# Optimization experiments

Hardware: AMD Instinct MI355X
Metric: run time of the kernel (lower is better)

## Reference

```python
import jax, jax.numpy as jnp
import numpy as np

H = 1024   # hidden_size
NH = 16    # num heads
DH = H // NH
L = 2      # attention levels
E = 8      # experts
F = 4 * H  # expert FFN hidden
B = 2
S = 1024
EPS = 1e-5
TOPK = 2
STD = 0.02


def setup_inputs() -> dict:
    key = jax.random.key(0)
    ks = jax.random.split(key, 12)
    def n(k, shp):
        return jax.random.normal(k, shp, jnp.float32) * STD
    return {
        "hidden_states": jax.random.normal(ks[0], (B, S, H), jnp.float32),
        "attention_mask": jnp.ones((B, S), jnp.int32),
        "ln1_g": jnp.ones((H,), jnp.float32), "ln1_b": jnp.zeros((H,), jnp.float32),
        "ln2_g": jnp.ones((H,), jnp.float32), "ln2_b": jnp.zeros((H,), jnp.float32),
        "Wq": n(ks[1], (L, H, H)), "Wk": n(ks[2], (L, H, H)),
        "Wv": n(ks[3], (L, H, H)), "Wo": n(ks[4], (L, H, H)),
        "bq": jnp.zeros((L, H), jnp.float32), "bk": jnp.zeros((L, H), jnp.float32),
        "bv": jnp.zeros((L, H), jnp.float32), "bo": jnp.zeros((L, H), jnp.float32),
        "level_logits": n(ks[5], (L,)),
        "Wr": n(ks[6], (H, E)), "br": jnp.zeros((E,), jnp.float32),
        "W1": n(ks[7], (E, H, F)), "b1": jnp.zeros((E, F), jnp.float32),
        "W2": n(ks[8], (E, F, H)), "b2": jnp.zeros((E, H), jnp.float32),
    }


def _ln(x, g, b):
    m = x.mean(-1, keepdims=True)
    v = x.var(-1, keepdims=True)
    return (x - m) * jax.lax.rsqrt(v + EPS) * g + b


def _mla(x, mask_f, Wq, Wk, Wv, Wo, bq, bk, bv, bo, level_logits):
    # Multi-level attention: one MHA per level, softmax-combined over levels.
    b_, s_, _ = x.shape
    def proj(W, bias):
        y = jnp.einsum('bsh,lhd->lbsd', x, W) + bias[:, None, None, :]
        return y.reshape(L, b_, s_, NH, DH)
    q, k, v = proj(Wq, bq), proj(Wk, bk), proj(Wv, bv)
    scores = jnp.einsum('lbqnd,lbknd->lbnqk', q, k) / np.float32(np.sqrt(DH))
    bias = (1.0 - mask_f)[None, :, None, None, :] * jnp.float32(-1e9)  # key-side mask
    attn = jax.nn.softmax(scores + bias, axis=-1)
    ctx = jnp.einsum('lbnqk,lbknd->lbqnd', attn, v).reshape(L, b_, s_, H)
    out = jnp.einsum('lbsh,lhd->lbsd', ctx, Wo) + bo[:, None, None, :]
    w = jax.nn.softmax(level_logits)
    return jnp.einsum('l,lbsd->bsd', w, out)


def _moe(x, Wr, br, W1, b1, W2, b2):
    # Top-2 softmax router with renormalized gates; dense expert compute,
    # sparse combine (math-equivalent to dispatch/combine without dropping).
    logits = x @ Wr + br                                  # [B,S,E]
    probs = jax.nn.softmax(logits, axis=-1)
    topv, topi = jax.lax.top_k(probs, TOPK)               # [B,S,K]
    gates = topv / topv.sum(-1, keepdims=True)
    combine = jnp.sum(jax.nn.one_hot(topi, E, dtype=x.dtype) * gates[..., None], axis=-2)  # [B,S,E]
    h = jax.nn.gelu(jnp.einsum('bsh,ehf->besf', x, W1) + b1[None, :, None, :])
    y = jnp.einsum('besf,efh->besh', h, W2) + b2[None, :, None, :]
    return jnp.einsum('bse,besh->bsh', combine, y), logits


def reference(hidden_states, attention_mask, ln1_g, ln1_b, ln2_g, ln2_b,
              Wq, Wk, Wv, Wo, bq, bk, bv, bo, level_logits,
              Wr, br, W1, b1, W2, b2):
    mask_f = attention_mask.astype(jnp.float32)
    attn = _mla(_ln(hidden_states, ln1_g, ln1_b), mask_f,
                Wq, Wk, Wv, Wo, bq, bk, bv, bo, level_logits)
    x = hidden_states + attn                  # residual 1 (dropout in eval = identity)
    moe_out, _router_logits = _moe(_ln(x, ln2_g, ln2_b), Wr, br, W1, b1, W2, b2)
    return x + moe_out                        # residual 2
```

## Files before the change

kernel.cpp:

```cpp
#include <hip/hip_runtime.h>
#include <hip/hip_bf16.h>
#include <stdint.h>

#define Hn   1024
#define NHn  16
#define DHn  64
#define Ln   2
#define En   8
#define Fn   4096
#define Bn   2
#define Sn   1024
#define Tn   2048
#define An   4096
#define KSPLIT 4

typedef __bf16 bf16_t;
typedef __bf16 bf16x2 __attribute__((ext_vector_type(2)));
typedef __bf16 bf16x4 __attribute__((ext_vector_type(4)));
typedef __bf16 bf16x8 __attribute__((ext_vector_type(8)));
typedef float  f32x4  __attribute__((ext_vector_type(4)));

__device__ __forceinline__ f32x4 mfma16(bf16x8 a, bf16x8 b, f32x4 c){
  return __builtin_amdgcn_mfma_f32_16x16x32_bf16(a, b, c, 0, 0, 0);
}
__device__ __forceinline__ void gload16(const void* gsrc, void* ldst){
  __builtin_amdgcn_global_load_lds((const __attribute__((address_space(1))) void*)gsrc,
                                   (__attribute__((address_space(3))) void*)ldst, 16, 0, 0);
}
__device__ __forceinline__ float gelu_f(float x){
  float u = 0.7978845608028654f * (x + 0.044715f * x * x * x);
  return 0.5f * x * (1.0f + tanhf(u));
}

__global__ __launch_bounds__(256)
void tcvt_k(const float* __restrict__ src, bf16_t* __restrict__ dst, int R, int C){
  __shared__ float tile[64][68];
  size_t moff = (size_t)blockIdx.z * R * C;
  src += moff; dst += moff;
  int c0 = blockIdx.x * 64, r0 = blockIdx.y * 64;
  int tid = threadIdx.x;
  int tx = tid & 15, ty = tid >> 4;
  #pragma unroll
  for (int i = 0; i < 4; ++i){
    float4 v = *(const float4*)(src + (size_t)(r0 + ty + i*16) * C + c0 + tx*4);
    *(float4*)&tile[ty + i*16][tx*4] = v;
  }
  __syncthreads();
  int c = tid >> 2, rq = tid & 3;
  #pragma unroll
  for (int i = 0; i < 2; ++i){
    int rr = (rq + i*4) * 8;
    bf16x8 pk;
    #pragma unroll
    for (int j = 0; j < 8; ++j) pk[j] = (bf16_t)tile[rr + j][c];
    *(bf16x8*)(dst + (size_t)(c0 + c) * R + r0 + rr) = pk;
  }
}

__global__ __launch_bounds__(256)
void ln_k(const float* __restrict__ x, const float* __restrict__ gam,
          const float* __restrict__ bet, bf16_t* __restrict__ out){
  int row = blockIdx.x;
  const float4* xr = (const float4*)(x + (size_t)row * Hn);
  int t = threadIdx.x, lane = t & 63, w = t >> 6;
  float4 v = xr[t];
  float s  = v.x + v.y + v.z + v.w;
  float ss = v.x*v.x + v.y*v.y + v.z*v.z + v.w*v.w;
  #pragma unroll
  for (int mk = 1; mk < 64; mk <<= 1){ s += __shfl_xor(s, mk); ss += __shfl_xor(ss, mk); }
  __shared__ float r1[4], r2[4];
  if (lane == 0){ r1[w] = s; r2[w] = ss; }
  __syncthreads();
  float S1 = r1[0]+r1[1]+r1[2]+r1[3];
  float S2 = r2[0]+r2[1]+r2[2]+r2[3];
  float mean = S1 * (1.0f/Hn);
  float var  = S2 * (1.0f/Hn) - mean*mean;
  float rstd = rsqrtf(var + 1e-5f);
  int c = t * 4;
  bf16_t* o = out + (size_t)row * Hn + c;
  o[0] = (bf16_t)((v.x-mean)*rstd*gam[c+0] + bet[c+0]);
  o[1] = (bf16_t)((v.y-mean)*rstd*gam[c+1] + bet[c+1]);
  o[2] = (bf16_t)((v.z-mean)*rstd*gam[c+2] + bet[c+2]);
  o[3] = (bf16_t)((v.w-mean)*rstd*gam[c+3] + bet[c+3]);
}

__global__ __launch_bounds__(256)
void res_ln2_k(const float* __restrict__ x, const float* __restrict__ o0,
               const float* __restrict__ o1, const float* __restrict__ lvl,
               const float* __restrict__ gam, const float* __restrict__ bet,
               float* __restrict__ x2, bf16_t* __restrict__ xn2){
  int row = blockIdx.x, t = threadIdx.x, lane = t & 63, w = t >> 6;
  float l0 = lvl[0], l1 = lvl[1];
  float mx = fmaxf(l0, l1);
  float e0 = __expf(l0 - mx), e1 = __expf(l1 - mx);
  float inv = 1.f / (e0 + e1);
  float w0 = e0 * inv, w1 = e1 * inv;
  size_t base = (size_t)row * Hn;
  float4 xv = ((const float4*)(x  + base))[t];
  float4 a0 = ((const float4*)(o0 + base))[t];
  float4 a1 = ((const float4*)(o1 + base))[t];
  float4 v;
  v.x = xv.x + w0*a0.x + w1*a1.x;
  v.y = xv.y + w0*a0.y + w1*a1.y;
  v.z = xv.z + w0*a0.z + w1*a1.z;
  v.w = xv.w + w0*a0.w + w1*a1.w;
  ((float4*)(x2 + base))[t] = v;
  float s  = v.x + v.y + v.z + v.w;
  float ss = v.x*v.x + v.y*v.y + v.z*v.z + v.w*v.w;
  #pragma unroll
  for (int mk = 1; mk < 64; mk <<= 1){ s += __shfl_xor(s, mk); ss += __shfl_xor(ss, mk); }
  __shared__ float r1[4], r2[4];
  if (lane == 0){ r1[w] = s; r2[w] = ss; }
  __syncthreads();
  float S1 = r1[0]+r1[1]+r1[2]+r1[3];
  float S2 = r2[0]+r2[1]+r2[2]+r2[3];
  float mean = S1 * (1.0f/Hn);
  float var  = S2 * (1.0f/Hn) - mean*mean;
  float rstd = rsqrtf(var + 1e-5f);
  int c = t * 4;
  bf16_t* o = xn2 + base + c;
  o[0] = (bf16_t)((v.x-mean)*rstd*gam[c+0] + bet[c+0]);
  o[1] = (bf16_t)((v.y-mean)*rstd*gam[c+1] + bet[c+1]);
  o[2] = (bf16_t)((v.z-mean)*rstd*gam[c+2] + bet[c+2]);
  o[3] = (bf16_t)((v.w-mean)*rstd*gam[c+3] + bet[c+3]);
}

struct GP {
  const bf16_t* A;
  const bf16_t* Bt;
  const float*  bias;
  float*        fout;
  bf16_t*       bfout;
  const int*    list;
  const int*    counts;
  int Kstride;
  int Kloc;
};

template<int MODE>
__global__ __launch_bounds__(256)
void gemm_k(GP p){
  const int nt = blockIdx.x, mt = blockIdx.y, z = blockIdx.z;
  const bf16_t* A = p.A;
  const bf16_t* Bt = p.Bt;
  const float* bias = p.bias;
  if constexpr (MODE == 0){
    Bt += (size_t)z*Hn*Hn; bias += z*Hn;
  } else {
    Bt += (size_t)z*Hn*Hn; bias += z*Hn; A += (size_t)z*Bn*Sn*Hn;
  }
  const int Ks = p.Kstride;
  const int NT = p.Kloc >> 5;

  __shared__ bf16_t As[2][128*32];
  __shared__ bf16_t Bs[2][128*32];
  const int tid = threadIdx.x, lane = tid & 63, w = tid >> 6;
  const int wr = (w >> 1) * 64, wc = (w & 1) * 64;
  const int lane15 = lane & 15, kg = lane >> 4;

  const bf16_t* aptr[2];
  const bf16_t* bptr[2];
  #pragma unroll
  for (int i = 0; i < 2; ++i){
    int ch = tid + i*256;
    int row = ch >> 2, kc = (ch & 3) * 8;
    aptr[i] = A  + (size_t)(mt*128 + row) * Ks + kc;
    bptr[i] = Bt + (size_t)(nt*128 + row) * Ks + kc;
  }

  const f32x4 fz = {0.f,0.f,0.f,0.f};
  f32x4 acc[4][4];
  #pragma unroll
  for (int m = 0; m < 4; ++m)
    #pragma unroll
    for (int n = 0; n < 4; ++n) acc[m][n] = fz;

  #pragma unroll
  for (int i = 0; i < 2; ++i){
    gload16(aptr[i], &As[0][(tid + i*256)*8]);
    gload16(bptr[i], &Bs[0][(tid + i*256)*8]);
  }
  __syncthreads();

  int cur = 0;
  for (int t = 0; t < NT; ++t){
    if (t + 1 < NT){
      int k1 = (t+1) * 32;
      #pragma unroll
      for (int i = 0; i < 2; ++i){
        gload16(aptr[i] + k1, &As[cur^1][(tid + i*256)*8]);
        gload16(bptr[i] + k1, &Bs[cur^1][(tid + i*256)*8]);
      }
    }
    bf16x8 af[4], bfr[4];
    #pragma unroll
    for (int m = 0; m < 4; ++m) af[m]  = *(const bf16x8*)(&As[cur][(wr + m*16 + lane15)*32 + kg*8]);
    #pragma unroll
    for (int n = 0; n < 4; ++n)  bfr[n] = *(const bf16x8*)(&Bs[cur][(wc + n*16 + lane15)*32 + kg*8]);
    #pragma unroll
    for (int m = 0; m < 4; ++m)
      #pragma unroll
      for (int n = 0; n < 4; ++n)
        acc[m][n] = mfma16(af[m], bfr[n], acc[m][n]);
    __syncthreads();
    cur ^= 1;
  }

  if constexpr (MODE == 0){
    bf16_t* outp = p.bfout + (size_t)z * (Bn*NHn*Sn*DHn);
    if (z < 4){
      #pragma unroll
      for (int m = 0; m < 4; ++m){
        int row0 = mt*128 + wr + m*16 + kg*4;
        #pragma unroll
        for (int n = 0; n < 4; ++n){
          int col = nt*128 + wc + n*16 + lane15;
          int nh = col >> 6, dh = col & 63;
          float bv = bias[col];
          f32x4 v = acc[m][n];
          #pragma unroll
          for (int r = 0; r < 4; ++r){
            int tk = row0 + r;
            int bb = tk >> 10, s = tk & 1023;
            outp[((size_t)(bb*NHn + nh)*Sn + s)*DHn + dh] = (bf16_t)(v[r] + bv);
          }
        }
      }
    } else {
      #pragma unroll
      for (int m = 0; m < 4; ++m){
        int row0 = mt*128 + wr + m*16 + kg*4;
        int bb = row0 >> 10, s = row0 & 1023;
        #pragma unroll
        for (int n = 0; n < 4; ++n){
          int col = nt*128 + wc + n*16 + lane15;
          int nh = col >> 6, dh = col & 63;
          float bv = bias[col];
          f32x4 v = acc[m][n];
          bf16x4 pk;
          pk[0] = (bf16_t)(v[0] + bv);
          pk[1] = (bf16_t)(v[1] + bv);
          pk[2] = (bf16_t)(v[2] + bv);
          pk[3] = (bf16_t)(v[3] + bv);
          *(bf16x4*)(outp + ((size_t)(bb*NHn + nh)*DHn + dh)*Sn + s) = pk;
        }
      }
    }
  } else {
    float* outp = p.fout + (size_t)z * Tn * Hn;
    #pragma unroll
    for (int m = 0; m < 4; ++m){
      int row0 = mt*128 + wr + m*16 + kg*4;
      #pragma unroll
      for (int n = 0; n < 4; ++n){
        int col = nt*128 + wc + n*16 + lane15;
        float bv = bias[col];
        f32x4 v = acc[m][n];
        #pragma unroll
        for (int r = 0; r < 4; ++r)
          outp[(size_t)(row0 + r)*Hn + col] = v[r] + bv;
      }
    }
  }
}

template<int MODE>
__global__ __launch_bounds__(256)
void moe_k(GP p){
  constexpr int NGRP = (MODE == 3) ? 2 : 4;
  constexpr int NTW  = (MODE == 3) ? 16 : 8;
  const int bid = blockIdx.x;
  const int x = bid & 7;
  const int tid = threadIdx.x, lane = tid & 63, w = tid >> 6;
  const int lane15 = lane & 15, kg = lane >> 4;
  const int wr = (w >> 1) * 64, wc = (w & 1) * 64;
  __shared__ bf16_t As[2][128*32];
  __shared__ bf16_t Bs[2][128*32];
  const f32x4 fz = {0.f,0.f,0.f,0.f};

  int colTotal = 0;
  #pragma unroll
  for (int m2 = 0; m2 < NGRP; ++m2){
    int gq = x + m2*8;
    int eq = (MODE == 3) ? (gq >> 1) : (gq >> 2);
    colTotal += ((p.counts[eq] + 127) >> 7) * NTW;
  }

  for (int j = bid >> 3; j < colTotal; j += 160){
    int rem = j, g = -1;
    #pragma unroll
    for (int m2 = 0; m2 < NGRP; ++m2){
      int gq = x + m2*8;
      int eq = (MODE == 3) ? (gq >> 1) : (gq >> 2);
      int ng = ((p.counts[eq] + 127) >> 7) * NTW;
      if (g < 0){ if (rem < ng) g = gq; else rem -= ng; }
    }
    int e, ks, mt, nt;
    if constexpr (MODE == 3){
      e = g >> 1; ks = 0;
      mt = rem >> 4; nt = ((g & 1) << 4) | (rem & 15);
    } else {
      e = g >> 2; ks = g & 3;
      mt = rem >> 3; nt = rem & 7;
    }
    const int cnt = p.counts[e];
    const int* list = p.list + e * Tn;
    int off = 0;
    #pragma unroll
    for (int q = 0; q < En; ++q){ if (q < e) off += p.counts[q]; }

    const int Ks    = (MODE == 3) ? Hn : Fn;
    const int kbase = (MODE == 3) ? 0 : ks * (Fn / KSPLIT);
    const bf16_t* Bt = p.Bt + (size_t)e * Fn * Hn;
    const float* bias = p.bias + ((MODE == 3) ? e*Fn : e*Hn);

    const bf16_t* aptr[2];
    const bf16_t* bptr[2];
    #pragma unroll
    for (int i = 0; i < 2; ++i){
      int ch = tid + i*256;
      int row = ch >> 2, kc = (ch & 3) * 8;
      int gi = mt*128 + row; if (gi >= cnt) gi = cnt - 1;
      int ar = (MODE == 3) ? (list[gi] >> 1) : (off + gi);
      aptr[i] = p.A + (size_t)ar * Ks + kbase + kc;
      bptr[i] = Bt + (size_t)(nt*128 + row) * Ks + kbase + kc;
    }

    f32x4 acc[4][4];
    #pragma unroll
    for (int m = 0; m < 4; ++m)
      #pragma unroll
      for (int n = 0; n < 4; ++n) acc[m][n] = fz;

    #pragma unroll
    for (int i = 0; i < 2; ++i){
      gload16(aptr[i], &As[0][(tid + i*256)*8]);
      gload16(bptr[i], &Bs[0][(tid + i*256)*8]);
    }
    __syncthreads();

    int cur = 0;
    for (int t = 0; t < 32; ++t){
      if (t + 1 < 32){
        int k1 = (t+1) * 32;
        #pragma unroll
        for (int i = 0; i < 2; ++i){
          gload16(aptr[i] + k1, &As[cur^1][(tid + i*256)*8]);
          gload16(bptr[i] + k1, &Bs[cur^1][(tid + i*256)*8]);
        }
      }
      bf16x8 af[4], bfr[4];
      #pragma unroll
      for (int m = 0; m < 4; ++m) af[m]  = *(const bf16x8*)(&As[cur][(wr + m*16 + lane15)*32 + kg*8]);
      #pragma unroll
      for (int n = 0; n < 4; ++n)  bfr[n] = *(const bf16x8*)(&Bs[cur][(wc + n*16 + lane15)*32 + kg*8]);
      #pragma unroll
      for (int m = 0; m < 4; ++m)
        #pragma unroll
        for (int n = 0; n < 4; ++n)
          acc[m][n] = mfma16(af[m], bfr[n], acc[m][n]);
      __syncthreads();
      cur ^= 1;
    }

    if constexpr (MODE == 3){
      #pragma unroll
      for (int m = 0; m < 4; ++m){
        int row0 = mt*128 + wr + m*16 + kg*4;
        #pragma unroll
        for (int n = 0; n < 4; ++n){
          int col = nt*128 + wc + n*16 + lane15;
          float bv = bias[col];
          f32x4 v = acc[m][n];
          #pragma unroll
          for (int r = 0; r < 4; ++r){
            int gi = row0 + r;
            if (gi < cnt)
              p.bfout[(size_t)(off + gi)*Fn + col] = (bf16_t)gelu_f(v[r] + bv);
          }
        }
      }
    } else {
      bf16_t* outp = p.bfout + (size_t)ks * An * Hn;
      bool addb = (ks == 0);
      #pragma unroll
      for (int m = 0; m < 4; ++m){
        int row0 = mt*128 + wr + m*16 + kg*4;
        #pragma unroll
        for (int n = 0; n < 4; ++n){
          int col = nt*128 + wc + n*16 + lane15;
          float bv = addb ? bias[col] : 0.f;
          f32x4 v = acc[m][n];
          #pragma unroll
          for (int r = 0; r < 4; ++r){
            int gi = row0 + r;
            if (gi < cnt){
              int aid = list[gi];
              outp[(size_t)aid*Hn + col] = (bf16_t)(v[r] + bv);
            }
          }
        }
      }
    }
  }
}

__global__ __launch_bounds__(256)
void attn_k(const bf16_t* __restrict__ qh, const bf16_t* __restrict__ kh,
            const bf16_t* __restrict__ vtb, const int* __restrict__ amask,
            bf16_t* __restrict__ ctxb){
  int z  = blockIdx.x;
  int qb = blockIdx.y;
  int lvl = z >> 5, bb = (z >> 4) & 1, nh = z & 15;
  int tid = threadIdx.x, lane = tid & 63, w = tid >> 6;
  int lane15 = lane & 15, kg = lane >> 4;
  const bf16_t* Q  = qh  + (size_t)z * Sn * DHn;
  const bf16_t* Kp = kh  + (size_t)z * Sn * DHn;
  const bf16_t* Vt = vtb + (size_t)z * DHn * Sn;
  const int* mrow = amask + bb * Sn;
  __shared__ bf16_t Ks[2][32*64];
  __shared__ bf16_t Vs[2][64*32];
  __shared__ float bias_lds[Sn];
  __shared__ bf16_t p_lds[4][16*40];
  {
    int4 mv = ((const int4*)mrow)[tid];
    float4 bv;
    bv.x = mv.x ? 0.f : -1e9f;
    bv.y = mv.y ? 0.f : -1e9f;
    bv.z = mv.z ? 0.f : -1e9f;
    bv.w = mv.w ? 0.f : -1e9f;
    ((float4*)bias_lds)[tid] = bv;
  }
  int krow = w*8 + (lane >> 3);
  const bf16_t* ksrc = Kp + (size_t)krow*DHn + (((lane&7) ^ (krow&7)) << 3);
  int vrow = w*16 + (lane >> 2);
  const bf16_t* vsrc = Vt + (size_t)vrow*Sn + ((((lane&3) ^ ((vrow>>2)&3))) << 3);
  bf16_t* kdst[2] = { &Ks[0][w*512 + lane*8], &Ks[1][w*512 + lane*8] };
  bf16_t* vdst[2] = { &Vs[0][w*512 + lane*8], &Vs[1][w*512 + lane*8] };

  const f32x4 fz = {0.f,0.f,0.f,0.f};
  int qt = qb*4 + w;
  int qr = qt*16 + lane15;
  bf16x8 qa0 = *(const bf16x8*)(Q + (size_t)qr*DHn + kg*8);
  bf16x8 qa1 = *(const bf16x8*)(Q + (size_t)qr*DHn + 32 + kg*8);
  f32x4 ctxa[4] = {fz, fz, fz, fz};
  float m_ln = -1e30f;
  float s_ln = 0.f;
  float m_out[4] = {-1e30f,-1e30f,-1e30f,-1e30f};

  const int kslot0 = (kg ^ (lane15 & 7));
  const int kslot1 = ((kg + 4) ^ (lane15 & 7));
  const int ka_off0 = lane15*64 + kslot0*8;
  const int ka_off1 = lane15*64 + kslot1*8;
  const int kb_off0 = (16 + lane15)*64 + kslot0*8;
  const int kb_off1 = (16 + lane15)*64 + kslot1*8;

  gload16(ksrc, kdst[0]);
  gload16(vsrc, vdst[0]);
  __syncthreads();

  for (int kc = 0; kc < 32; ++kc){
    const int cur = kc & 1;
    const bf16_t* Kb = Ks[cur];
    const bf16_t* Vb = Vs[cur];
    if (kc + 1 < 32){
      gload16(ksrc + (size_t)(kc+1)*32*DHn, kdst[cur^1]);
      gload16(vsrc + (kc+1)*32,             vdst[cur^1]);
    }
    int k0 = kc * 32;
    bf16x8 ka0 = *(const bf16x8*)(Kb + ka_off0);
    bf16x8 ka1 = *(const bf16x8*)(Kb + ka_off1);
    bf16x8 kb0 = *(const bf16x8*)(Kb + kb_off0);
    bf16x8 kb1 = *(const bf16x8*)(Kb + kb_off1);
    f32x4 sA = mfma16(ka1, qa1, mfma16(ka0, qa0, fz));
    f32x4 sB = mfma16(kb1, qa1, mfma16(kb0, qa0, fz));
    float4 biasA = *(const float4*)(bias_lds + k0 + kg*4);
    float4 biasB = *(const float4*)(bias_lds + k0 + 16 + kg*4);
    float sv[8];
    sv[0] = sA[0]*0.125f + biasA.x;
    sv[1] = sA[1]*0.125f + biasA.y;
    sv[2] = sA[2]*0.125f + biasA.z;
    sv[3] = sA[3]*0.125f + biasA.w;
    sv[4] = sB[0]*0.125f + biasB.x;
    sv[5] = sB[1]*0.125f + biasB.y;
    sv[6] = sB[2]*0.125f + biasB.z;
    sv[7] = sB[3]*0.125f + biasB.w;
    float mx = fmaxf(fmaxf(fmaxf(sv[0],sv[1]),fmaxf(sv[2],sv[3])),
                     fmaxf(fmaxf(sv[4],sv[5]),fmaxf(sv[6],sv[7])));
    mx = fmaxf(mx, __shfl_xor(mx, 16));
    mx = fmaxf(mx, __shfl_xor(mx, 32));
    if (!__all(mx <= m_ln)){
      float mnew = fmaxf(m_ln, mx);
      s_ln *= __expf(m_ln - mnew);
      #pragma unroll
      for (int r = 0; r < 4; ++r){
        float mo = __shfl(mnew, kg*4 + r);
        float corr = __expf(m_out[r] - mo);
        ctxa[0][r] *= corr; ctxa[1][r] *= corr; ctxa[2][r] *= corr; ctxa[3][r] *= corr;
        m_out[r] = mo;
      }
      m_ln = mnew;
    }
    float pv[8];
    #pragma unroll
    for (int j = 0; j < 8; ++j){ pv[j] = __expf(sv[j] - m_ln); s_ln += pv[j]; }
    bf16_t* pr = p_lds[w] + lane15*40;
    *(bf16x2*)(pr + kg*4)          = (bf16x2){(bf16_t)pv[0], (bf16_t)pv[1]};
    *(bf16x2*)(pr + kg*4 + 2)      = (bf16x2){(bf16_t)pv[2], (bf16_t)pv[3]};
    *(bf16x2*)(pr + 16 + kg*4)     = (bf16x2){(bf16_t)pv[4], (bf16_t)pv[5]};
    *(bf16x2*)(pr + 16 + kg*4 + 2) = (bf16x2){(bf16_t)pv[6], (bf16_t)pv[7]};
    bf16x8 paf = *(const bf16x8*)(p_lds[w] + lane15*40 + kg*8);
    #pragma unroll
    for (int df = 0; df < 4; ++df){
      int r = df*16 + lane15;
      bf16x8 vbf = *(const bf16x8*)(Vb + r*32 + ((kg ^ ((r>>2)&3)) << 3));
      ctxa[df] = mfma16(paf, vbf, ctxa[df]);
    }
    __syncthreads();
  }
  s_ln += __shfl_xor(s_ln, 16);
  s_ln += __shfl_xor(s_ln, 32);
  #pragma unroll
  for (int r = 0; r < 4; ++r){
    float inv = 1.f / __shfl(s_ln, kg*4 + r);
    int srow = qt*16 + kg*4 + r;
    #pragma unroll
    for (int df = 0; df < 4; ++df){
      int d = df*16 + lane15;
      ctxb[((size_t)(lvl*2 + bb)*Sn + srow)*Hn + nh*DHn + d] = (bf16_t)(ctxa[df][r] * inv);
    }
  }
}

__global__ __launch_bounds__(64)
void router_k(const float* __restrict__ x2, const float* __restrict__ gam,
              const float* __restrict__ bet, const float* __restrict__ Wr,
              const float* __restrict__ br, float* __restrict__ gates,
              int* __restrict__ lists, int* __restrict__ counts){
  int t = blockIdx.x, lane = threadIdx.x;
  const float4* xr = (const float4*)(x2 + (size_t)t * Hn);
  float4 vbuf[4];
  float s = 0.f, ss = 0.f;
  #pragma unroll
  for (int i = 0; i < 4; ++i){
    float4 v = xr[lane + i*64];
    vbuf[i] = v;
    s  += v.x + v.y + v.z + v.w;
    ss += v.x*v.x + v.y*v.y + v.z*v.z + v.w*v.w;
  }
  #pragma unroll
  for (int mk = 1; mk < 64; mk <<= 1){ s += __shfl_xor(s, mk); ss += __shfl_xor(ss, mk); }
  float mean = s * (1.0f/Hn);
  float var  = ss * (1.0f/Hn) - mean*mean;
  float rstd = rsqrtf(var + 1e-5f);
  float a[8] = {0,0,0,0,0,0,0,0};
  #pragma unroll
  for (int i = 0; i < 4; ++i){
    int c = (lane + i*64) * 4;
    float4 v = vbuf[i];
    float xn[4] = {
      (v.x-mean)*rstd*gam[c+0] + bet[c+0],
      (v.y-mean)*rstd*gam[c+1] + bet[c+1],
      (v.z-mean)*rstd*gam[c+2] + bet[c+2],
      (v.w-mean)*rstd*gam[c+3] + bet[c+3]};
    #pragma unroll
    for (int j = 0; j < 4; ++j){
      const float* w = Wr + (size_t)(c + j) * En;
      #pragma unroll
      for (int e8 = 0; e8 < 8; ++e8) a[e8] += xn[j] * w[e8];
    }
  }
  #pragma unroll
  for (int e8 = 0; e8 < 8; ++e8)
    #pragma unroll
    for (int mk = 1; mk < 64; mk <<= 1) a[e8] += __shfl_xor(a[e8], mk);
  if (lane == 0){
    float lg[8]; float mx = -1e30f;
    #pragma unroll
    for (int e8 = 0; e8 < 8; ++e8){ lg[e8] = a[e8] + br[e8]; mx = fmaxf(mx, lg[e8]); }
    float p[8];
    #pragma unroll
    for (int e8 = 0; e8 < 8; ++e8) p[e8] = __expf(lg[e8] - mx);
    int i0 = 0; float v0 = p[0];
    #pragma unroll
    for (int e8 = 1; e8 < 8; ++e8) if (p[e8] > v0){ v0 = p[e8]; i0 = e8; }
    int i1 = -1; float v1 = -1.f;
    #pragma unroll
    for (int e8 = 0; e8 < 8; ++e8) if (e8 != i0 && p[e8] > v1){ v1 = p[e8]; i1 = e8; }
    float g0 = v0 / (v0 + v1), g1 = v1 / (v0 + v1);
    gates[2*t] = g0; gates[2*t+1] = g1;
    int s0 = atomicAdd(&counts[i0], 1); lists[i0*Tn + s0] = 2*t;
    int s1 = atomicAdd(&counts[i1], 1); lists[i1*Tn + s1] = 2*t + 1;
  }
}

__global__ __launch_bounds__(256)
void comb_k(const float* __restrict__ x2, const bf16_t* __restrict__ P,
            const float* __restrict__ gates, float* __restrict__ out){
  int t = blockIdx.x, i = threadIdx.x;
  float g0 = gates[2*t], g1 = gates[2*t+1];
  const size_t PS = (size_t)An * Hn;
  f32x4 s0 = {0,0,0,0}, s1 = {0,0,0,0};
  #pragma unroll
  for (int ks = 0; ks < KSPLIT; ++ks){
    bf16x4 u0 = *(const bf16x4*)(P + ks*PS + (size_t)(2*t)*Hn + i*4);
    bf16x4 u1 = *(const bf16x4*)(P + ks*PS + (size_t)(2*t+1)*Hn + i*4);
    #pragma unroll
    for (int j = 0; j < 4; ++j){ s0[j] += (float)u0[j]; s1[j] += (float)u1[j]; }
  }
  f32x4 va = ((const f32x4*)(x2 + (size_t)t*Hn))[i];
  f32x4 o = va + g0*s0 + g1*s1;
  ((f32x4*)(out + (size_t)t*Hn))[i] = o;
}

extern "C" void kernel_launch(void* const* d_in, const int* in_sizes, int n_in,
                              void* d_out, int out_size, void* d_ws, size_t ws_size,
                              hipStream_t stream)
{
  const float* x    = (const float*)d_in[0];
  const int* amask  = (const int*)d_in[1];
  const float* ln1g = (const float*)d_in[2];
  const float* ln1b = (const float*)d_in[3];
  const float* ln2g = (const float*)d_in[4];
  const float* ln2b = (const float*)d_in[5];
  const float* Wq   = (const float*)d_in[6];
  const float* Wk   = (const float*)d_in[7];
  const float* Wv   = (const float*)d_in[8];
  const float* Wo   = (const float*)d_in[9];
  const float* bq   = (const float*)d_in[10];
  const float* bk   = (const float*)d_in[11];
  const float* bv   = (const float*)d_in[12];
  const float* bo   = (const float*)d_in[13];
  const float* lvl  = (const float*)d_in[14];
  const float* Wr   = (const float*)d_in[15];
  const float* br   = (const float*)d_in[16];
  const float* W1   = (const float*)d_in[17];
  const float* b1   = (const float*)d_in[18];
  const float* W2   = (const float*)d_in[19];
  const float* b2   = (const float*)d_in[20];
  float* out = (float*)d_out;
  (void)in_sizes; (void)n_in; (void)out_size; (void)ws_size;

  char* wsp = (char*)d_ws;
  auto nxt = [&](size_t bytes) -> char* {
    char* r = wsp; wsp += (bytes + 255) & ~(size_t)255; return r;
  };
  bf16_t* wqkvT = (bf16_t*)nxt((size_t)6*Hn*Hn*2);
  bf16_t* woT   = (bf16_t*)nxt((size_t)Ln*Hn*Hn*2);
  bf16_t* w1t   = (bf16_t*)nxt((size_t)En*Fn*Hn*2);
  bf16_t* w2t   = (bf16_t*)nxt((size_t)En*Hn*Fn*2);
  float*  bqkv  = (float*)nxt((size_t)6*Hn*4);
  bf16_t* xn1   = (bf16_t*)nxt((size_t)Tn*Hn*2);
  bf16_t* qkvh  = (bf16_t*)nxt((size_t)6*Bn*NHn*Sn*DHn*2);
  bf16_t* ctxb  = (bf16_t*)nxt((size_t)Ln*Bn*Sn*Hn*2);
  float*  otmp  = (float*)nxt((size_t)Ln*Tn*Hn*4);
  float*  x2    = (float*)nxt((size_t)Tn*Hn*4);
  bf16_t* xn2   = (bf16_t*)nxt((size_t)Tn*Hn*2);
  float*  gates = (float*)nxt((size_t)Tn*2*4);
  int*    lists = (int*)nxt((size_t)En*Tn*4);
  int*    counts= (int*)nxt(256);
  bf16_t* hbuf  = (bf16_t*)nxt((size_t)An*Fn*2);
  bf16_t* ybuf  = (bf16_t*)nxt((size_t)KSPLIT*An*Hn*2);

  hipMemsetAsync(counts, 0, En*sizeof(int), stream);
  hipMemcpyAsync(bqkv,          bq, (size_t)Ln*Hn*4, hipMemcpyDeviceToDevice, stream);
  hipMemcpyAsync(bqkv + 2*Hn,   bk, (size_t)Ln*Hn*4, hipMemcpyDeviceToDevice, stream);
  hipMemcpyAsync(bqkv + 4*Hn,   bv, (size_t)Ln*Hn*4, hipMemcpyDeviceToDevice, stream);

  tcvt_k<<<dim3(16,16,Ln), 256, 0, stream>>>(Wq, wqkvT,            Hn, Hn);
  tcvt_k<<<dim3(16,16,Ln), 256, 0, stream>>>(Wk, wqkvT + 2*Hn*Hn,  Hn, Hn);
  tcvt_k<<<dim3(16,16,Ln), 256, 0, stream>>>(Wv, wqkvT + 4*Hn*Hn,  Hn, Hn);
  tcvt_k<<<dim3(16,16,Ln), 256, 0, stream>>>(Wo, woT,              Hn, Hn);
  tcvt_k<<<dim3(Fn/64, Hn/64, En), 256, 0, stream>>>(W1, w1t, Hn, Fn);
  tcvt_k<<<dim3(Hn/64, Fn/64, En), 256, 0, stream>>>(W2, w2t, Fn, Hn);

  ln_k<<<Tn, 256, 0, stream>>>(x, ln1g, ln1b, xn1);

  { GP g{};
    g.A = xn1; g.Bt = wqkvT; g.bias = bqkv; g.bfout = qkvh;
    g.Kstride = Hn; g.Kloc = Hn;
    gemm_k<0><<<dim3(8,16,6), 256, 0, stream>>>(g); }

  {
    const bf16_t* qh = qkvh;
    const bf16_t* kh = qkvh + (size_t)2*Bn*NHn*Sn*DHn;
    const bf16_t* vt = qkvh + (size_t)4*Bn*NHn*Sn*DHn;
    attn_k<<<dim3(Ln*Bn*NHn, Sn/64), 256, 0, stream>>>(qh, kh, vt, amask, ctxb);
  }

  { GP g{};
    g.A = ctxb; g.Bt = woT; g.bias = bo; g.fout = otmp;
    g.Kstride = Hn; g.Kloc = Hn;
    gemm_k<1><<<dim3(8,16,2), 256, 0, stream>>>(g); }

  res_ln2_k<<<Tn, 256, 0, stream>>>(x, otmp, otmp + (size_t)Tn*Hn, lvl,
                                    ln2g, ln2b, x2, xn2);
  router_k<<<Tn, 64, 0, stream>>>(x2, ln2g, ln2b, Wr, br, gates, lists, counts);

  { GP g{};
    g.A = xn2; g.Bt = w1t; g.bias = b1; g.bfout = hbuf;
    g.list = lists; g.counts = counts;
    moe_k<3><<<dim3(1280,1,1), 256, 0, stream>>>(g); }
  { GP g{};
    g.A = hbuf; g.Bt = w2t; g.bfout = ybuf; g.bias = b2;
    g.list = lists; g.counts = counts;
    moe_k<4><<<dim3(1280,1,1), 256, 0, stream>>>(g); }

  comb_k<<<Tn, 256, 0, stream>>>(x2, ybuf, gates, out);
}
```

Measured before the change: 520.0 us.

## Rewrite MoE expert GEMMs with 256x256 tiles, 512 threads and swizzled LDS

Replaces the persistent 128x128-tile MoE GEMM kernel with a one-tile-per-block kernel using 256x256 output tiles, 8 waves, a K-step of 64, and an XOR-swizzled shared-memory layout to avoid bank conflicts. Larger tiles raise arithmetic intensity and cut global reloads of weights and activations. Blocks are indexed directly per expert, and blocks with no work exit early. In exchange it uses 128 KB of LDS per block and 128 accumulator registers per thread, which limits occupancy, and it wastes more padding work when an expert's token count is not a multiple of 256.

```diff
diff --git a/kernel.cpp b/kernel.cpp
--- a/kernel.cpp
+++ b/kernel.cpp
@@ -265,139 +265,129 @@
 }
 
 template<int MODE>
-__global__ __launch_bounds__(256)
-void moe_k(GP p){
-  constexpr int NGRP = (MODE == 3) ? 2 : 4;
-  constexpr int NTW  = (MODE == 3) ? 16 : 8;
-  const int bid = blockIdx.x;
-  const int x = bid & 7;
-  const int tid = threadIdx.x, lane = tid & 63, w = tid >> 6;
+__global__ __launch_bounds__(512)
+void moe256_k(GP p){
+  const int e = blockIdx.x & 7;
+  const int j = blockIdx.x >> 3;
+  const int cnt = p.counts[e];
+  const int mtiles = (cnt + 255) >> 8;
+  if (j >= mtiles * 16) return;
+  int mt, nt, ks;
+  if constexpr (MODE == 3){
+    mt = j >> 4; nt = j & 15; ks = 0;
+  } else {
+    mt = j >> 4; int r2 = j & 15; ks = r2 >> 2; nt = r2 & 3;
+  }
+  const int* list = p.list + e * Tn;
+  int off = 0;
+  #pragma unroll
+  for (int q = 0; q < En; ++q) off += (q < e) ? p.counts[q] : 0;
+
+  const int Ks    = (MODE == 3) ? Hn : Fn;
+  const int kbase = (MODE == 3) ? 0 : ks * (Fn / KSPLIT);
+  const int NKT   = 16;
+  const bf16_t* Bt = p.Bt + (size_t)e * Fn * Hn;
+  const float* bias = p.bias + ((MODE == 3) ? e*Fn : e*Hn);
+
+  __shared__ bf16_t As[2][256*64];
+  __shared__ bf16_t Bs[2][256*64];
+
+  const int tid = threadIdx.x, lane = tid & 63;
+  const int w = tid >> 6, wm = w >> 2, wn = w & 3;
   const int lane15 = lane & 15, kg = lane >> 4;
-  const int wr = (w >> 1) * 64, wc = (w & 1) * 64;
-  __shared__ bf16_t As[2][128*32];
-  __shared__ bf16_t Bs[2][128*32];
+
+  const bf16_t* asrc[4];
+  const bf16_t* bsrc[4];
+  int cofs[4];
+  #pragma unroll
+  for (int i = 0; i < 4; ++i){
+    int c = tid + i*512;
+    cofs[i] = c;
+    int row = c >> 3, s = c & 7;
+    int kcol = ((s ^ (row & 7)) << 3);
+    int gi = mt*256 + row; if (gi >= cnt) gi = cnt - 1;
+    int ar = (MODE == 3) ? (list[gi] >> 1) : (off + gi);
+    asrc[i] = p.A + (size_t)ar * Ks + kbase + kcol;
+    bsrc[i] = Bt + (size_t)(nt*256 + row) * Ks + kbase + kcol;
+  }
+
   const f32x4 fz = {0.f,0.f,0.f,0.f};
-
-  int colTotal = 0;
-  #pragma unroll
-  for (int m2 = 0; m2 < NGRP; ++m2){
-    int gq = x + m2*8;
-    int eq = (MODE == 3) ? (gq >> 1) : (gq >> 2);
-    colTotal += ((p.counts[eq] + 127) >> 7) * NTW;
-  }
-
-  for (int j = bid >> 3; j < colTotal; j += 160){
-    int rem = j, g = -1;
-    #pragma unroll
-    for (int m2 = 0; m2 < NGRP; ++m2){
-      int gq = x + m2*8;
-      int eq = (MODE == 3) ? (gq >> 1) : (gq >> 2);
-      int ng = ((p.counts[eq] + 127) >> 7) * NTW;
-      if (g < 0){ if (rem < ng) g = gq; else rem -= ng; }
-    }
-    int e, ks, mt, nt;
-    if constexpr (MODE == 3){
-      e = g >> 1; ks = 0;
-      mt = rem >> 4; nt = ((g & 1) << 4) | (rem & 15);
-    } else {
-      e = g >> 2; ks = g & 3;
-      mt = rem >> 3; nt = rem & 7;
-    }
-    const int cnt = p.counts[e];
-    const int* list = p.list + e * Tn;
-    int off = 0;
-    #pragma unroll
-    for (int q = 0; q < En; ++q){ if (q < e) off += p.counts[q]; }
-
-    const int Ks    = (MODE == 3) ? Hn : Fn;
-    const int kbase = (MODE == 3) ? 0 : ks * (Fn / KSPLIT);
-    const bf16_t* Bt = p.Bt + (size_t)e * Fn * Hn;
-    const float* bias = p.bias + ((MODE == 3) ? e*Fn : e*Hn);
-
-    const bf16_t* aptr[2];
-    const bf16_t* bptr[2];
-    #pragma unroll
-    for (int i = 0; i < 2; ++i){
-      int ch = tid + i*256;
-      int row = ch >> 2, kc = (ch & 3) * 8;
-      int gi = mt*128 + row; if (gi >= cnt) gi = cnt - 1;
-      int ar = (MODE == 3) ? (list[gi] >> 1) : (off + gi);
-      aptr[i] = p.A + (size_t)ar * Ks + kbase + kc;
-      bptr[i] = Bt + (size_t)(nt*128 + row) * Ks + kbase + kc;
-    }
-
-    f32x4 acc[4][4];
-    #pragma unroll
-    for (int m = 0; m < 4; ++m)
-      #pragma unroll
-      for (int n = 0; n < 4; ++n) acc[m][n] = fz;
-
-    #pragma unroll
-    for (int i = 0; i < 2; ++i){
-      gload16(aptr[i], &As[0][(tid + i*256)*8]);
-      gload16(bptr[i], &Bs[0][(tid + i*256)*8]);
+  f32x4 acc[8][4];
+  #pragma unroll
+  for (int m = 0; m < 8; ++m)
+    #pragma unroll
+    for (int n = 0; n < 4; ++n) acc[m][n] = fz;
+
+  #pragma unroll
+  for (int i = 0; i < 4; ++i){
+    gload16(asrc[i], &As[0][cofs[i]*8]);
+    gload16(bsrc[i], &Bs[0][cofs[i]*8]);
+  }
+  __syncthreads();
+
+  const int sbase = lane15 & 7;
+  for (int kt = 0; kt < NKT; ++kt){
+    const int cur = kt & 1;
+    if (kt + 1 < NKT){
+      int k1 = (kt+1) * 64;
+      #pragma unroll
+      for (int i = 0; i < 4; ++i){
+        gload16(asrc[i] + k1, &As[cur^1][cofs[i]*8]);
+        gload16(bsrc[i] + k1, &Bs[cur^1][cofs[i]*8]);
+      }
+    }
+    #pragma unroll
+    for (int ks2 = 0; ks2 < 2; ++ks2){
+      const int sl = (((ks2*4 + kg) ^ sbase) << 3);
+      bf16x8 bfr[4];
+      #pragma unroll
+      for (int nf = 0; nf < 4; ++nf)
+        bfr[nf] = *(const bf16x8*)(&Bs[cur][(wn*64 + nf*16 + lane15)*64 + sl]);
+      #pragma unroll
+      for (int mf = 0; mf < 8; ++mf){
+        bf16x8 af = *(const bf16x8*)(&As[cur][(wm*128 + mf*16 + lane15)*64 + sl]);
+        #pragma unroll
+        for (int nf = 0; nf < 4; ++nf)
+          acc[mf][nf] = mfma16(af, bfr[nf], acc[mf][nf]);
+      }
     }
     __syncthreads();
-
-    int cur = 0;
-    for (int t = 0; t < 32; ++t){
-      if (t + 1 < 32){
-        int k1 = (t+1) * 32;
+  }
+
+  if constexpr (MODE == 3){
+    #pragma unroll
+    for (int mf = 0; mf < 8; ++mf){
+      int row0 = mt*256 + wm*128 + mf*16 + kg*4;
+      #pragma unroll
+      for (int nf = 0; nf < 4; ++nf){
+        int col = nt*256 + wn*64 + nf*16 + lane15;
+        float bv = bias[col];
+        f32x4 v = acc[mf][nf];
         #pragma unroll
-        for (int i = 0; i < 2; ++i){
-          gload16(aptr[i] + k1, &As[cur^1][(tid + i*256)*8]);
-          gload16(bptr[i] + k1, &Bs[cur^1][(tid + i*256)*8]);
+        for (int r = 0; r < 4; ++r){
+          int gi = row0 + r;
+          if (gi < cnt)
+            p.bfout[(size_t)(off + gi)*Fn + col] = (bf16_t)gelu_f(v[r] + bv);
         }
       }
-      bf16x8 af[4], bfr[4];
-      #pragma unroll
-      for (int m = 0; m < 4; ++m) af[m]  = *(const bf16x8*)(&As[cur][(wr + m*16 + lane15)*32 + kg*8]);
-      #pragma unroll
-      for (int n = 0; n < 4; ++n)  bfr[n] = *(const bf16x8*)(&Bs[cur][(wc + n*16 + lane15)*32 + kg*8]);
-      #pragma unroll
-      for (int m = 0; m < 4; ++m)
+    }
+  } else {
+    bf16_t* outp = p.bfout + (size_t)ks * An * Hn;
+    bool addb = (ks == 0);
+    #pragma unroll
+    for (int mf = 0; mf < 8; ++mf){
+      int row0 = mt*256 + wm*128 + mf*16 + kg*4;
+      #pragma unroll
+      for (int nf = 0; nf < 4; ++nf){
+        int col = nt*256 + wn*64 + nf*16 + lane15;
+        float bv = addb ? bias[col] : 0.f;
+        f32x4 v = acc[mf][nf];
         #pragma unroll
-        for (int n = 0; n < 4; ++n)
-          acc[m][n] = mfma16(af[m], bfr[n], acc[m][n]);
-      __syncthreads();
-      cur ^= 1;
-    }
-
-    if constexpr (MODE == 3){
-      #pragma unroll
-      for (int m = 0; m < 4; ++m){
-        int row0 = mt*128 + wr + m*16 + kg*4;
-        #pragma unroll
-        for (int n = 0; n < 4; ++n){
-          int col = nt*128 + wc + n*16 + lane15;
-          float bv = bias[col];
-          f32x4 v = acc[m][n];
-          #pragma unroll
-          for (int r = 0; r < 4; ++r){
-            int gi = row0 + r;
-            if (gi < cnt)
-              p.bfout[(size_t)(off + gi)*Fn + col] = (bf16_t)gelu_f(v[r] + bv);
-          }
-        }
-      }
-    } else {
-      bf16_t* outp = p.bfout + (size_t)ks * An * Hn;
-      bool addb = (ks == 0);
-      #pragma unroll
-      for (int m = 0; m < 4; ++m){
-        int row0 = mt*128 + wr + m*16 + kg*4;
-        #pragma unroll
-        for (int n = 0; n < 4; ++n){
-          int col = nt*128 + wc + n*16 + lane15;
-          float bv = addb ? bias[col] : 0.f;
-          f32x4 v = acc[m][n];
-          #pragma unroll
-          for (int r = 0; r < 4; ++r){
-            int gi = row0 + r;
-            if (gi < cnt){
-              int aid = list[gi];
-              outp[(size_t)aid*Hn + col] = (bf16_t)(v[r] + bv);
-            }
+        for (int r = 0; r < 4; ++r){
+          int gi = row0 + r;
+          if (gi < cnt){
+            int aid = list[gi];
+            outp[(size_t)aid*Hn + col] = (bf16_t)(v[r] + bv);
           }
         }
       }
@@ -700,11 +690,11 @@
   { GP g{};
     g.A = xn2; g.Bt = w1t; g.bias = b1; g.bfout = hbuf;
     g.list = lists; g.counts = counts;
-    moe_k<3><<<dim3(1280,1,1), 256, 0, stream>>>(g); }
+    moe256_k<3><<<dim3(1024,1,1), 512, 0, stream>>>(g); }
   { GP g{};
     g.A = hbuf; g.Bt = w2t; g.bfout = ybuf; g.bias = b2;
     g.list = lists; g.counts = counts;
-    moe_k<4><<<dim3(1280,1,1), 256, 0, stream>>>(g); }
+    moe256_k<4><<<dim3(1024,1,1), 512, 0, stream>>>(g); }
 
   comb_k<<<Tn, 256, 0, stream>>>(x2, ybuf, gates, out);
 }
```

After: 518.2 us. Within noise of the previous version (-0.3%).

## Replace persistent MoE GEMM loop with static grid and deeper split-K

Applied to the files above, without the earlier changes.

The MoE expert GEMM kernels drop the persistent grid-stride loop and its per-iteration work-lookup scan. Each block now maps directly to one (expert, M-tile, N-tile, k-split) tile, and blocks past an expert's token count exit early. The second GEMM's split-K factor doubles, giving more parallel blocks with shorter K loops. The cost is more partial-sum output that the combine step must write, read and reduce. Correctness also depends on the output buffer and the combine kernel handling the larger split count.

```diff
diff --git a/kernel.cpp b/kernel.cpp
--- a/kernel.cpp
+++ b/kernel.cpp
@@ -12,7 +12,7 @@
 #define Sn   1024
 #define Tn   2048
 #define An   4096
-#define KSPLIT 4
+#define KSPLIT 8
 
 typedef __bf16 bf16_t;
 typedef __bf16 bf16x2 __attribute__((ext_vector_type(2)));
@@ -267,137 +267,123 @@
 template<int MODE>
 __global__ __launch_bounds__(256)
 void moe_k(GP p){
-  constexpr int NGRP = (MODE == 3) ? 2 : 4;
-  constexpr int NTW  = (MODE == 3) ? 16 : 8;
   const int bid = blockIdx.x;
-  const int x = bid & 7;
-  const int tid = threadIdx.x, lane = tid & 63, w = tid >> 6;
-  const int lane15 = lane & 15, kg = lane >> 4;
-  const int wr = (w >> 1) * 64, wc = (w & 1) * 64;
+  const int x = bid & 7, r = bid >> 3;
+  int e, mt, nt, ks;
+  if constexpr (MODE == 3){
+    int slot = r >> 8, j = r & 255;
+    int g = slot*8 + x;
+    e = g >> 1; ks = 0;
+    mt = j >> 4;
+    nt = ((g & 1) << 4) | (j & 15);
+  } else {
+    int slot = r >> 7, j = r & 127;
+    e = slot; ks = x;
+    mt = j >> 3; nt = j & 7;
+  }
+  const int cnt = p.counts[e];
+  if (mt * 128 >= cnt) return;
+  const int* list = p.list + e * Tn;
+  int off = 0;
+  #pragma unroll
+  for (int q = 0; q < En; ++q) off += (q < e) ? p.counts[q] : 0;
+
+  const int Ks    = (MODE == 3) ? Hn : Fn;
+  const int kbase = (MODE == 3) ? 0 : ks * (Fn / KSPLIT);
+  const int NT    = (MODE == 3) ? 32 : (Fn / KSPLIT) / 32;
+  const bf16_t* Bt = p.Bt + (size_t)e * Fn * Hn;
+  const float* bias = p.bias + ((MODE == 3) ? e*Fn : e*Hn);
+
   __shared__ bf16_t As[2][128*32];
   __shared__ bf16_t Bs[2][128*32];
+  const int tid = threadIdx.x, lane = tid & 63, w = tid >> 6;
+  const int wr = (w >> 1) * 64, wc = (w & 1) * 64;
+  const int lane15 = lane & 15, kg = lane >> 4;
+
+  const bf16_t* aptr[2];
+  const bf16_t* bptr[2];
+  #pragma unroll
+  for (int i = 0; i < 2; ++i){
+    int ch = tid + i*256;
+    int row = ch >> 2, kc = (ch & 3) * 8;
+    int gi = mt*128 + row; if (gi >= cnt) gi = cnt - 1;
+    int ar = (MODE == 3) ? (list[gi] >> 1) : (off + gi);
+    aptr[i] = p.A + (size_t)ar * Ks + kbase + kc;
+    bptr[i] = Bt + (size_t)(nt*128 + row) * Ks + kbase + kc;
+  }
+
   const f32x4 fz = {0.f,0.f,0.f,0.f};
-
-  int colTotal = 0;
-  #pragma unroll
-  for (int m2 = 0; m2 < NGRP; ++m2){
-    int gq = x + m2*8;
-    int eq = (MODE == 3) ? (gq >> 1) : (gq >> 2);
-    colTotal += ((p.counts[eq] + 127) >> 7) * NTW;
-  }
-
-  for (int j = bid >> 3; j < colTotal; j += 160){
-    int rem = j, g = -1;
-    #pragma unroll
-    for (int m2 = 0; m2 < NGRP; ++m2){
-      int gq = x + m2*8;
-      int eq = (MODE == 3) ? (gq >> 1) : (gq >> 2);
-      int ng = ((p.counts[eq] + 127) >> 7) * NTW;
-      if (g < 0){ if (rem < ng) g = gq; else rem -= ng; }
-    }
-    int e, ks, mt, nt;
-    if constexpr (MODE == 3){
-      e = g >> 1; ks = 0;
-      mt = rem >> 4; nt = ((g & 1) << 4) | (rem & 15);
-    } else {
-      e = g >> 2; ks = g & 3;
-      mt = rem >> 3; nt = rem & 7;
-    }
-    const int cnt = p.counts[e];
-    const int* list = p.list + e * Tn;
-    int off = 0;
-    #pragma unroll
-    for (int q = 0; q < En; ++q){ if (q < e) off += p.counts[q]; }
-
-    const int Ks    = (MODE == 3) ? Hn : Fn;
-    const int kbase = (MODE == 3) ? 0 : ks * (Fn / KSPLIT);
-    const bf16_t* Bt = p.Bt + (size_t)e * Fn * Hn;
-    const float* bias = p.bias + ((MODE == 3) ? e*Fn : e*Hn);
-
-    const bf16_t* aptr[2];
-    const bf16_t* bptr[2];
-    #pragma unroll
-    for (int i = 0; i < 2; ++i){
-      int ch = tid + i*256;
-      int row = ch >> 2, kc = (ch & 3) * 8;
-      int gi = mt*128 + row; if (gi >= cnt) gi = cnt - 1;
-      int ar = (MODE == 3) ? (list[gi] >> 1) : (off + gi);
-      aptr[i] = p.A + (size_t)ar * Ks + kbase + kc;
-      bptr[i] = Bt + (size_t)(nt*128 + row) * Ks + kbase + kc;
-    }
-
-    f32x4 acc[4][4];
+  f32x4 acc[4][4];
+  #pragma unroll
+  for (int m = 0; m < 4; ++m)
+    #pragma unroll
+    for (int n = 0; n < 4; ++n) acc[m][n] = fz;
+
+  #pragma unroll
+  for (int i = 0; i < 2; ++i){
+    gload16(aptr[i], &As[0][(tid + i*256)*8]);
+    gload16(bptr[i], &Bs[0][(tid + i*256)*8]);
+  }
+  __syncthreads();
+
+  int cur = 0;
+  for (int t = 0; t < NT; ++t){
+    if (t + 1 < NT){
+      int k1 = (t+1) * 32;
+      #pragma unroll
+      for (int i = 0; i < 2; ++i){
+        gload16(aptr[i] + k1, &As[cur^1][(tid + i*256)*8]);
+        gload16(bptr[i] + k1, &Bs[cur^1][(tid + i*256)*8]);
+      }
+    }
+    bf16x8 af[4], bfr[4];
+    #pragma unroll
+    for (int m = 0; m < 4; ++m) af[m]  = *(const bf16x8*)(&As[cur][(wr + m*16 + lane15)*32 + kg*8]);
+    #pragma unroll
+    for (int n = 0; n < 4; ++n)  bfr[n] = *(const bf16x8*)(&Bs[cur][(wc + n*16 + lane15)*32 + kg*8]);
     #pragma unroll
     for (int m = 0; m < 4; ++m)
       #pragma unroll
-      for (int n = 0; n < 4; ++n) acc[m][n] = fz;
-
-    #pragma unroll
-    for (int i = 0; i < 2; ++i){
-      gload16(aptr[i], &As[0][(tid + i*256)*8]);
-      gload16(bptr[i], &Bs[0][(tid + i*256)*8]);
-    }
+      for (int n = 0; n < 4; ++n)
+        acc[m][n] = mfma16(af[m], bfr[n], acc[m][n]);
     __syncthreads();
-
-    int cur = 0;
-    for (int t = 0; t < 32; ++t){
-      if (t + 1 < 32){
-        int k1 = (t+1) * 32;
+    cur ^= 1;
+  }
+
+  if constexpr (MODE == 3){
+    #pragma unroll
+    for (int m = 0; m < 4; ++m){
+      int row0 = mt*128 + wr + m*16 + kg*4;
+      #pragma unroll
+      for (int n = 0; n < 4; ++n){
+        int col = nt*128 + wc + n*16 + lane15;
+        float bv = bias[col];
+        f32x4 v = acc[m][n];
         #pragma unroll
-        for (int i = 0; i < 2; ++i){
-          gload16(aptr[i] + k1, &As[cur^1][(tid + i*256)*8]);
-          gload16(bptr[i] + k1, &Bs[cur^1][(tid + i*256)*8]);
+        for (int r = 0; r < 4; ++r){
+          int gi = row0 + r;
+          if (gi < cnt)
+            p.bfout[(size_t)(off + gi)*Fn + col] = (bf16_t)gelu_f(v[r] + bv);
         }
       }
-      bf16x8 af[4], bfr[4];
-      #pragma unroll
-      for (int m = 0; m < 4; ++m) af[m]  = *(const bf16x8*)(&As[cur][(wr + m*16 + lane15)*32 + kg*8]);
-      #pragma unroll
-      for (int n = 0; n < 4; ++n)  bfr[n] = *(const bf16x8*)(&Bs[cur][(wc + n*16 + lane15)*32 + kg*8]);
-      #pragma unroll
-      for (int m = 0; m < 4; ++m)
+    }
+  } else {
+    bf16_t* outp = p.bfout + (size_t)ks * An * Hn;
+    bool addb = (ks == 0);
+    #pragma unroll
+    for (int m = 0; m < 4; ++m){
+      int row0 = mt*128 + wr + m*16 + kg*4;
+      #pragma unroll
+      for (int n = 0; n < 4; ++n){
+        int col = nt*128 + wc + n*16 + lane15;
+        float bv = addb ? bias[col] : 0.f;
+        f32x4 v = acc[m][n];
         #pragma unroll
-        for (int n = 0; n < 4; ++n)
-          acc[m][n] = mfma16(af[m], bfr[n], acc[m][n]);
-      __syncthreads();
-      cur ^= 1;
-    }
-
-    if constexpr (MODE == 3){
-      #pragma unroll
-      for (int m = 0; m < 4; ++m){
-        int row0 = mt*128 + wr + m*16 + kg*4;
-        #pragma unroll
-        for (int n = 0; n < 4; ++n){
-          int col = nt*128 + wc + n*16 + lane15;
-          float bv = bias[col];
-          f32x4 v = acc[m][n];
-          #pragma unroll
-          for (int r = 0; r < 4; ++r){
-            int gi = row0 + r;
-            if (gi < cnt)
-              p.bfout[(size_t)(off + gi)*Fn + col] = (bf16_t)gelu_f(v[r] + bv);
-          }
-        }
-      }
-    } else {
-      bf16_t* outp = p.bfout + (size_t)ks * An * Hn;
-      bool addb = (ks == 0);
-      #pragma unroll
-      for (int m = 0; m < 4; ++m){
-        int row0 = mt*128 + wr + m*16 + kg*4;
-        #pragma unroll
-        for (int n = 0; n < 4; ++n){
-          int col = nt*128 + wc + n*16 + lane15;
-          float bv = addb ? bias[col] : 0.f;
-          f32x4 v = acc[m][n];
-          #pragma unroll
-          for (int r = 0; r < 4; ++r){
-            int gi = row0 + r;
-            if (gi < cnt){
-              int aid = list[gi];
-              outp[(size_t)aid*Hn + col] = (bf16_t)(v[r] + bv);
-            }
+        for (int r = 0; r < 4; ++r){
+          int gi = row0 + r;
+          if (gi < cnt){
+            int aid = list[gi];
+            outp[(size_t)aid*Hn + col] = (bf16_t)(v[r] + bv);
           }
         }
       }
@@ -700,11 +686,11 @@
   { GP g{};
     g.A = xn2; g.Bt = w1t; g.bias = b1; g.bfout = hbuf;
     g.list = lists; g.counts = counts;
-    moe_k<3><<<dim3(1280,1,1), 256, 0, stream>>>(g); }
+    moe_k<3><<<dim3(4096,1,1), 256, 0, stream>>>(g); }
   { GP g{};
     g.A = hbuf; g.Bt = w2t; g.bfout = ybuf; g.bias = b2;
     g.list = lists; g.counts = counts;
-    moe_k<4><<<dim3(1280,1,1), 256, 0, stream>>>(g); }
+    moe_k<4><<<dim3(8192,1,1), 256, 0, stream>>>(g); }
 
   comb_k<<<Tn, 256, 0, stream>>>(x2, ybuf, gates, out);
 }
```

Measured after the change: 514.0 us. About the same (-1.2%).
